# Kernel optimization log

Hardware: AMD Instinct MI355X
Metric: run time of the kernel (lower is better)

The kernel has to match this reference:

```python
import jax, jax.numpy as jnp
import numpy as np

H, W = 512, 512          # pseudo_image_dims
C = 32                   # feat_channels == MHA embed_dim
NH, HD = 2, 16           # heads, head_dim
B, NL, NR = 2, 50000, 20000
EPS = 1e-5
SCALE = np.float32(1.0 / np.sqrt(HD))

# 3x3 neighbor shifts used by shift_bev_grids (INDEX_SHIFT in source)
INDEX_SHIFT = jnp.array([[0, 0], [-1, 0], [1, 0], [0, 1], [-1, 1], [1, 1], [0, -1], [-1, -1], [1, -1]], dtype=jnp.int32)
# 5x5 shifts used by new_gen_dy_coor (gen_index_shift(2))
SHIFT25 = jnp.array([[i, j] for i in range(-2, 3) for j in range(-2, 3)], dtype=jnp.int32)


def _unique_coords(key, n):
    perm = jax.random.permutation(key, H * W)[:n]
    return jnp.stack([perm // W, perm % W], axis=1).astype(jnp.int32)


def setup_inputs():
    key = jax.random.key(0)
    ks = jax.random.split(key, 8)
    inp = {
        "li_bev_feats": jax.random.normal(ks[0], (B, NL, C), jnp.float32),
        "li_bev_coors": jnp.stack([_unique_coords(jax.random.fold_in(ks[1], b), NL) for b in range(B)]),
        "ra_bev_feats": jax.random.normal(ks[2], (B, NR, C), jnp.float32),
        "ra_bev_coors": jnp.stack([_unique_coords(jax.random.fold_in(ks[3], b), NR) for b in range(B)]),
        "radar_bev_dy": jax.random.bernoulli(ks[4], 0.3, (B, NR)),
    }
    pk = jax.random.split(ks[5], 12)
    w = lambda k, o, i: 0.05 * jax.random.normal(k, (o, i), jnp.float32)
    z = lambda n: jnp.zeros((n,), jnp.float32)
    inp.update(
        ln_li_w=jnp.ones((C,), jnp.float32), ln_li_b=z(C),
        ln_ra_w=jnp.ones((C,), jnp.float32), ln_ra_b=z(C),
        q1_w=w(pk[0], C, C), q1_b=z(C), k1_w=w(pk[1], C, C), k1_b=z(C), v1_w=w(pk[2], C, C), v1_b=z(C),
        q2_w=w(pk[3], C, C), q2_b=z(C), k2_w=w(pk[4], C, C), k2_b=z(C), v2_w=w(pk[5], C, C), v2_b=z(C),
        pos_w=w(pk[6], C, 2), pos_b=z(C),
        a1_in_w=w(pk[7], 3 * C, C), a1_in_b=z(3 * C), a1_out_w=w(pk[8], C, C), a1_out_b=z(C),
        a2_in_w=w(pk[9], 3 * C, C), a2_in_b=z(3 * C), a2_out_w=w(pk[10], C, C), a2_out_b=z(C),
    )
    return inp


def _ln(x, w, b):
    mu = jnp.mean(x, -1, keepdims=True)
    var = jnp.mean(jnp.square(x - mu), -1, keepdims=True)
    return (x - mu) / jnp.sqrt(var + EPS) * w + b


def _grid_of(coors, n):
    # dense coord -> pillar-index lookup table, -1 for empty cells
    return jnp.full((H, W), -1, jnp.int32).at[coors[:, 0], coors[:, 1]].set(jnp.arange(n, dtype=jnp.int32))


def _gather_kv(coors, grid, k_map, v_map, pe9):
    # per pillar: look up the 3x3 shifted neighbors in the OTHER modality's grid
    sh = coors[:, None, :] + INDEX_SHIFT[None]                      # [N,9,2]
    inb = (sh[..., 0] >= 0) & (sh[..., 0] < H) & (sh[..., 1] >= 0) & (sh[..., 1] < W)
    idx = grid[jnp.clip(sh[..., 0], 0, H - 1), jnp.clip(sh[..., 1], 0, W - 1)]
    valid = (inb & (idx >= 0))[..., None]                           # [N,9,1]
    safe = jnp.clip(idx, 0, None)
    k = jnp.where(valid, k_map[safe], 0.0)                          # masked_fill(~cond, 0)
    v = jnp.where(valid, v_map[safe] + pe9[None], 0.0)              # pos-enc added before masking
    return k, v


def _mha(q, k, v, Wi, bi, Wo, bo):
    # torch MultiheadAttention (batch_first, eval -> no dropout); q [N,1,C], k/v [N,9,C]
    n = q.shape[0]
    qp = (q @ Wi[:C].T + bi[:C]).reshape(n, 1, NH, HD)
    kp = (k @ Wi[C:2 * C].T + bi[C:2 * C]).reshape(n, -1, NH, HD)
    vp = (v @ Wi[2 * C:].T + bi[2 * C:]).reshape(n, -1, NH, HD)
    s = jnp.einsum("nqhd,nkhd->nhqk", qp, kp) * SCALE
    a = jax.nn.softmax(s, axis=-1)
    o = jnp.einsum("nhqk,nkhd->nqhd", a, vp).reshape(n, C)
    return o @ Wo.T + bo


def _scatter(coors, feat):
    # PointPillarsScatter: place [N,C] features at their (x,y) cells of a [C,H,W] canvas
    return jnp.zeros((H, W, C), feat.dtype).at[coors[:, 0], coors[:, 1]].set(feat).transpose(2, 0, 1)


def _forward(li_bev_feats, li_bev_coors, ra_bev_feats, ra_bev_coors, radar_bev_dy,
             ln_li_w, ln_li_b, ln_ra_w, ln_ra_b,
             q1_w, q1_b, k1_w, k1_b, v1_w, v1_b,
             q2_w, q2_b, k2_w, k2_b, v2_w, v2_b,
             pos_w, pos_b,
             a1_in_w, a1_in_b, a1_out_w, a1_out_b,
             a2_in_w, a2_in_b, a2_out_w, a2_out_b):
    pe9 = INDEX_SHIFT.astype(jnp.float32) @ pos_w.T + pos_b        # [9,C] positional codes

    def per_sample(li_f, li_c, ra_f, ra_c, ra_dy):
        li_n = _ln(li_f, ln_li_w, ln_li_b)
        ra_n = _ln(ra_f, ln_ra_w, ln_ra_b)
        li_grid = _grid_of(li_c, NL)
        ra_grid = _grid_of(ra_c, NR)
        # new_gen_dy_coor: lidar pillars within a 5x5 (mod dims+1) window of any dynamic radar pillar
        g = jnp.array([H + 1, W + 1], jnp.int32)
        sh = (ra_c[:, None, :] + SHIFT25[None]) % g                # [NR,25,2]
        inb = (sh[..., 0] < H) & (sh[..., 1] < W)
        idx = li_grid[jnp.clip(sh[..., 0], 0, H - 1), jnp.clip(sh[..., 1], 0, W - 1)]
        valid = inb & (idx >= 0) & ra_dy[:, None]
        dy_mask = jnp.zeros(NL + 1, bool).at[jnp.where(valid, idx, NL).reshape(-1)].set(True)[:NL]
        # branch 1: dynamic lidar queries cross-attend to 3x3 radar neighbors
        q1 = li_n @ q1_w.T + q1_b
        k1 = ra_n @ k1_w.T + k1_b
        v1 = ra_n @ v1_w.T + v1_b
        k, v = _gather_kv(li_c, ra_grid, k1, v1, pe9)
        out1 = _mha(q1[:, None, :], k, v, a1_in_w, a1_in_b, a1_out_w, a1_out_b)
        out1 = out1 * dy_mask[:, None].astype(out1.dtype)          # only dy pillars scattered
        img_li = _scatter(li_c, out1)
        # branch 2: radar queries cross-attend to 3x3 lidar neighbors
        q2 = ra_n @ q2_w.T + q2_b
        k2 = li_n @ k2_w.T + k2_b
        v2 = li_n @ v2_w.T + v2_b
        k, v = _gather_kv(ra_c, li_grid, k2, v2, pe9)
        out2 = _mha(q2[:, None, :], k, v, a2_in_w, a2_in_b, a2_out_w, a2_out_b)
        img_ra = _scatter(ra_c, out2)
        return img_li, img_ra

    return jax.vmap(per_sample)(li_bev_feats, li_bev_coors, ra_bev_feats, ra_bev_coors, radar_bev_dy)


def reference(li_bev_feats, li_bev_coors, ra_bev_feats, ra_bev_coors, radar_bev_dy,
              ln_li_w, ln_li_b, ln_ra_w, ln_ra_b,
              q1_w, q1_b, k1_w, k1_b, v1_w, v1_b,
              q2_w, q2_b, k2_w, k2_b, v2_w, v2_b,
              pos_w, pos_b,
              a1_in_w, a1_in_b, a1_out_w, a1_out_b,
              a2_in_w, a2_in_b, a2_out_w, a2_out_b):
    return _forward(li_bev_feats, li_bev_coors, ra_bev_feats, ra_bev_coors, radar_bev_dy,
                    ln_li_w, ln_li_b, ln_ra_w, ln_ra_b,
                    q1_w, q1_b, k1_w, k1_b, v1_w, v1_b,
                    q2_w, q2_b, k2_w, k2_b, v2_w, v2_b,
                    pos_w, pos_b,
                    a1_in_w, a1_in_b, a1_out_w, a1_out_b,
                    a2_in_w, a2_in_b, a2_out_w, a2_out_b)
```

## Files before the change

kernel.cpp:

```cpp
#include <hip/hip_runtime.h>
#include <stdint.h>

constexpr int Hh = 512, Ww = 512;
constexpr int HW = Hh * Ww;
constexpr int C  = 32;
constexpr int B  = 2;
constexpr int NL = 50000;
constexpr int NR = 20000;
constexpr float EPS = 1e-5f;
constexpr float SCALE = 0.25f;

constexpr int GBL = (NL + NR + 255) / 256;
constexpr int LB  = (NL + 255) / 256;
constexpr int RB  = (NR + 255) / 256;

constexpr int CB_MATS = 0;
constexpr int CB_CVEC = 6144;
constexpr int CB_PE1  = 6336;
constexpr int CB_PE2  = 6624;
constexpr int CB_INV  = 6912;
constexpr int CB_TOT  = 7040;

__device__ __constant__ int DX9[9] = {0,-1,1,0,-1,1,0,-1,1};
__device__ __constant__ int DY9[9] = {0,0,0,1,1,1,-1,-1,-1};

__global__ void setup_k(const int* __restrict__ li_c, const int* __restrict__ ra_c,
                        const int* __restrict__ ra_dy,
                        int* __restrict__ li_grid, int* __restrict__ ra_grid,
                        uint8_t* __restrict__ rdy_grid,
                        const float* __restrict__ a1w, const float* __restrict__ a1b,
                        const float* __restrict__ a2w, const float* __restrict__ a2b,
                        const float* __restrict__ q1w, const float* __restrict__ q1b,
                        const float* __restrict__ k1w, const float* __restrict__ k1b,
                        const float* __restrict__ v1w, const float* __restrict__ v1b,
                        const float* __restrict__ q2w, const float* __restrict__ q2b,
                        const float* __restrict__ k2w, const float* __restrict__ k2b,
                        const float* __restrict__ v2w, const float* __restrict__ v2b,
                        const float* __restrict__ posw, const float* __restrict__ posb,
                        float* __restrict__ cb) {
    int bx = blockIdx.x, b = blockIdx.y, t = threadIdx.x;
    if (bx < GBL) {
        int i = bx * 256 + t;
        if (i < NL) {
            int x = li_c[((size_t)b * NL + i) * 2 + 0];
            int y = li_c[((size_t)b * NL + i) * 2 + 1];
            li_grid[(size_t)b * HW + x * Ww + y] = i;
        } else if (i < NL + NR) {
            int j = i - NL;
            int x = ra_c[((size_t)b * NR + j) * 2 + 0];
            int y = ra_c[((size_t)b * NR + j) * 2 + 1];
            ra_grid[(size_t)b * HW + x * Ww + y] = j;
            if (ra_dy[(size_t)b * NR + j] != 0)
                rdy_grid[(size_t)b * HW + x * Ww + y] = 0;
        }
        return;
    }
    if (b != 0) return;
    if (bx < GBL + 6) {
        int m = bx - GBL;
        const float* A = (m < 3 ? a1w : a2w) + (m % 3) * C * C;
        const float* Wm;
        switch (m) { case 0: Wm=q1w; break; case 1: Wm=k1w; break; case 2: Wm=v1w; break;
                     case 3: Wm=q2w; break; case 4: Wm=k2w; break; default: Wm=v2w; }
        for (int p = t; p < 1024; p += 256) {
            int r = p >> 5, d = p & 31;
            float s = 0.f;
            #pragma unroll
            for (int c = 0; c < C; ++c) s += A[r * C + c] * Wm[c * C + d];
            cb[CB_MATS + m * 1024 + r * C + d] = s;
        }
        return;
    }
    for (int u = t; u < 896; u += 256) {
        if (u < 192) {
            int mm = u / 32, r = u & 31;
            const float* A  = (mm < 3 ? a1w : a2w) + (mm % 3) * C * C;
            const float* ab = (mm < 3 ? a1b : a2b) + (mm % 3) * C;
            const float* bv = (mm == 0 ? q1b : mm == 1 ? k1b : mm == 2 ? v1b
                             : mm == 3 ? q2b : mm == 4 ? k2b : v2b);
            float s = ab[r];
            #pragma unroll
            for (int c = 0; c < C; ++c) s += A[r * C + c] * bv[c];
            cb[CB_CVEC + mm * 32 + r] = s;
        } else if (u < 768) {
            int w = u - 192;
            int br = w / 288; int v = w % 288; int j = v >> 5, r = v & 31;
            const float* A = (br == 0 ? a1w : a2w) + 2 * C * C;
            float sx = (float)DX9[j], sy = (float)DY9[j];
            float s = 0.f;
            #pragma unroll
            for (int c = 0; c < C; ++c) {
                float pe = posw[c * 2 + 0] * sx + posw[c * 2 + 1] * sy + posb[c];
                s += A[r * C + c] * pe;
            }
            cb[(br == 0 ? CB_PE1 : CB_PE2) + j * 32 + r] = s;
        } else {
            int v = u - 768; int mm = v >> 5, r = v & 31;
            cb[CB_INV + v] = (mm == 0 ? a1b[32 + r] : mm == 1 ? a1b[64 + r]
                            : mm == 2 ? a2b[32 + r] : a2b[64 + r]);
        }
    }
}

__global__ void ln_proj_k(const float* __restrict__ li_f, const float* __restrict__ ra_f,
                          const float* __restrict__ ln_li_w, const float* __restrict__ ln_li_b,
                          const float* __restrict__ ln_ra_w, const float* __restrict__ ln_ra_b,
                          const float* __restrict__ cb,
                          float* __restrict__ qp1, float* __restrict__ kp2, float* __restrict__ vp2,
                          float* __restrict__ qp2, float* __restrict__ kp1, float* __restrict__ vp1) {
    bool lidar = (blockIdx.x < LB);
    int n  = lidar ? NL : NR;
    int i  = (lidar ? blockIdx.x : blockIdx.x - LB) * 256 + threadIdx.x;
    int b  = blockIdx.y;
    int mq = lidar ? 0 : 3, mk = lidar ? 4 : 1, mv = lidar ? 5 : 2;
    const float* feats = lidar ? li_f : ra_f;
    const float* lnw = lidar ? ln_li_w : ln_ra_w;
    const float* lnb = lidar ? ln_li_b : ln_ra_b;
    float* o0 = lidar ? qp1 : qp2;
    float* o1 = lidar ? kp2 : kp1;
    float* o2 = lidar ? vp2 : vp1;

    __shared__ float sM[3][1024];
    __shared__ float sc[3][32];
    for (int p = threadIdx.x; p < 1024; p += blockDim.x) {
        sM[0][p] = cb[CB_MATS + mq * 1024 + p];
        sM[1][p] = cb[CB_MATS + mk * 1024 + p];
        sM[2][p] = cb[CB_MATS + mv * 1024 + p];
    }
    if (threadIdx.x < 32) {
        sc[0][threadIdx.x] = cb[CB_CVEC + mq * 32 + threadIdx.x];
        sc[1][threadIdx.x] = cb[CB_CVEC + mk * 32 + threadIdx.x];
        sc[2][threadIdx.x] = cb[CB_CVEC + mv * 32 + threadIdx.x];
    }
    __syncthreads();
    if (i >= n) return;

    float x[C];
    const float4* f4 = (const float4*)(feats + ((size_t)b * n + i) * C);
    #pragma unroll
    for (int q = 0; q < 8; ++q) {
        float4 t = f4[q];
        x[4*q] = t.x; x[4*q+1] = t.y; x[4*q+2] = t.z; x[4*q+3] = t.w;
    }
    float mu = 0.f;
    #pragma unroll
    for (int c = 0; c < C; ++c) mu += x[c];
    mu *= (1.0f / C);
    float var = 0.f;
    #pragma unroll
    for (int c = 0; c < C; ++c) { float d = x[c] - mu; var += d * d; }
    var *= (1.0f / C);
    float inv = 1.0f / sqrtf(var + EPS);
    #pragma unroll
    for (int c = 0; c < C; ++c) x[c] = (x[c] - mu) * inv * lnw[c] + lnb[c];

    float* outs[3] = { o0, o1, o2 };
    #pragma unroll
    for (int m = 0; m < 3; ++m) {
        float4* o4 = (float4*)(outs[m] + ((size_t)b * n + i) * C);
        #pragma unroll
        for (int rq = 0; rq < 8; ++rq) {
            float4 t;
            float* tp = &t.x;
            #pragma unroll
            for (int rr = 0; rr < 4; ++rr) {
                int r = rq * 4 + rr;
                float s = sc[m][r];
                #pragma unroll
                for (int d = 0; d < C; ++d) s += sM[m][r * C + d] * x[d];
                tp[rr] = s;
            }
            o4[rq] = t;
        }
    }
}

__global__ void attn_k(const float* __restrict__ qp1, const float* __restrict__ kp1,
                       const float* __restrict__ vp1, const float* __restrict__ qp2,
                       const float* __restrict__ kp2, const float* __restrict__ vp2,
                       const int* __restrict__ li_c, const int* __restrict__ ra_c,
                       const int* __restrict__ li_grid, const int* __restrict__ ra_grid,
                       const uint8_t* __restrict__ rdy_grid, const float* __restrict__ cb,
                       const float* __restrict__ a1ow, const float* __restrict__ a1ob,
                       const float* __restrict__ a2ow, const float* __restrict__ a2ob,
                       float* __restrict__ feat1, float* __restrict__ feat2) {
    bool br1 = (blockIdx.x < LB);
    int nq  = br1 ? NL : NR;
    int nkv = br1 ? NR : NL;
    int i   = (br1 ? blockIdx.x : blockIdx.x - LB) * 256 + threadIdx.x;
    int b   = blockIdx.y;
    const float* qmap = br1 ? qp1 : qp2;
    const float* kmap = br1 ? kp1 : kp2;
    const float* vmap = br1 ? vp1 : vp2;
    const int* q_coors  = br1 ? li_c : ra_c;
    const int* kv_grid  = br1 ? ra_grid : li_grid;
    const float* Wo = br1 ? a1ow : a2ow;
    const float* bo = br1 ? a1ob : a2ob;
    int pe_off   = br1 ? CB_PE1 : CB_PE2;
    int kinv_off = br1 ? CB_INV + 0  : CB_INV + 64;
    int vinv_off = br1 ? CB_INV + 32 : CB_INV + 96;
    float* feat  = br1 ? feat1 : feat2;

    __shared__ float sWo[1024];
    __shared__ float sbo[32], skinv[32], svinv[32];
    __shared__ float spe[9 * 32];
    for (int p = threadIdx.x; p < 1024; p += blockDim.x) sWo[p] = Wo[p];
    if (threadIdx.x < 32) {
        sbo[threadIdx.x]   = bo[threadIdx.x];
        skinv[threadIdx.x] = cb[kinv_off + threadIdx.x];
        svinv[threadIdx.x] = cb[vinv_off + threadIdx.x];
    }
    for (int p = threadIdx.x; p < 288; p += blockDim.x) spe[p] = cb[pe_off + p];
    __syncthreads();

    if (i >= nq) return;
    float4* o4 = (float4*)(feat + ((size_t)b * nq + i) * C);

    int x = q_coors[((size_t)b * nq + i) * 2 + 0];
    int y = q_coors[((size_t)b * nq + i) * 2 + 1];

    if (br1) {
        bool dy = false;
        #pragma unroll
        for (int dx = -2; dx <= 2 && !dy; ++dx) {
            int cx = x + dx;
            cx = (cx < 0) ? cx + 513 : (cx >= 513 ? cx - 513 : cx);
            if (cx == 512) continue;
            #pragma unroll
            for (int dyy = -2; dyy <= 2; ++dyy) {
                int cy = y + dyy;
                cy = (cy < 0) ? cy + 513 : (cy >= 513 ? cy - 513 : cy);
                if (cy == 512) continue;
                if (rdy_grid[(size_t)b * HW + cx * Ww + cy] == 0) { dy = true; break; }
            }
        }
        if (!dy) {
            float4 z = {0.f, 0.f, 0.f, 0.f};
            #pragma unroll
            for (int q = 0; q < 8; ++q) o4[q] = z;
            return;
        }
    }

    int nidx[9];
    #pragma unroll
    for (int j = 0; j < 9; ++j) {
        int sx = x + DX9[j], sy = y + DY9[j];
        nidx[j] = (sx >= 0 && sx < Hh && sy >= 0 && sy < Ww)
                  ? kv_grid[(size_t)b * HW + sx * Ww + sy] : -1;
    }

    float qp[C];
    const float4* qp4 = (const float4*)(qmap + ((size_t)b * nq + i) * C);
    #pragma unroll
    for (int q = 0; q < 8; ++q) {
        float4 t = qp4[q];
        qp[4*q] = t.x; qp[4*q+1] = t.y; qp[4*q+2] = t.z; qp[4*q+3] = t.w;
    }

    float sc0[9], sc1[9];
    #pragma unroll
    for (int j = 0; j < 9; ++j) {
        int idx = nidx[j];
        const float4* kp4 = (idx >= 0) ? (const float4*)(kmap + ((size_t)b * nkv + idx) * C)
                                       : (const float4*)skinv;
        float s0 = 0.f, s1 = 0.f;
        #pragma unroll
        for (int q = 0; q < 4; ++q) {
            float4 t = kp4[q];
            s0 += qp[4*q] * t.x + qp[4*q+1] * t.y + qp[4*q+2] * t.z + qp[4*q+3] * t.w;
        }
        #pragma unroll
        for (int q = 4; q < 8; ++q) {
            float4 t = kp4[q];
            s1 += qp[4*q] * t.x + qp[4*q+1] * t.y + qp[4*q+2] * t.z + qp[4*q+3] * t.w;
        }
        sc0[j] = s0 * SCALE; sc1[j] = s1 * SCALE;
    }
    float m0 = sc0[0], m1 = sc1[0];
    #pragma unroll
    for (int j = 1; j < 9; ++j) { m0 = fmaxf(m0, sc0[j]); m1 = fmaxf(m1, sc1[j]); }
    float sum0 = 0.f, sum1 = 0.f;
    #pragma unroll
    for (int j = 0; j < 9; ++j) {
        sc0[j] = expf(sc0[j] - m0); sum0 += sc0[j];
        sc1[j] = expf(sc1[j] - m1); sum1 += sc1[j];
    }
    float r0 = 1.0f / sum0, r1 = 1.0f / sum1;

    float o[C];
    #pragma unroll
    for (int c = 0; c < C; ++c) o[c] = 0.f;
    #pragma unroll
    for (int j = 0; j < 9; ++j) {
        float a0 = sc0[j] * r0, a1 = sc1[j] * r1;
        int idx = nidx[j];
        if (idx >= 0) {
            const float4* vp4 = (const float4*)(vmap + ((size_t)b * nkv + idx) * C);
            #pragma unroll
            for (int q = 0; q < 8; ++q) {
                float4 t = vp4[q];
                float a = (q < 4) ? a0 : a1;
                o[4*q]   += a * (t.x + spe[j * 32 + 4*q]);
                o[4*q+1] += a * (t.y + spe[j * 32 + 4*q+1]);
                o[4*q+2] += a * (t.z + spe[j * 32 + 4*q+2]);
                o[4*q+3] += a * (t.w + spe[j * 32 + 4*q+3]);
            }
        } else {
            #pragma unroll
            for (int d = 0; d < 16; ++d) {
                o[d]      += a0 * svinv[d];
                o[16 + d] += a1 * svinv[16 + d];
            }
        }
    }

    #pragma unroll
    for (int rq = 0; rq < 8; ++rq) {
        float4 t;
        float* tp = &t.x;
        #pragma unroll
        for (int rr = 0; rr < 4; ++rr) {
            int r = rq * 4 + rr;
            float s = sbo[r];
            #pragma unroll
            for (int c = 0; c < C; ++c) s += sWo[r * C + c] * o[c];
            tp[rr] = s;
        }
        o4[rq] = t;
    }
}

__global__ void canvas_k(const int* __restrict__ li_grid, const int* __restrict__ ra_grid,
                         const float* __restrict__ feat1, const float* __restrict__ feat2,
                         float* __restrict__ out_li, float* __restrict__ out_ra) {
    int b = blockIdx.y;
    int cell = blockIdx.x * blockDim.x + threadIdx.x;
    if (cell >= HW) return;
    size_t gidx = (size_t)b * HW + cell;
    size_t obase = (size_t)b * C * HW + cell;

    int li = li_grid[gidx];
    float v[C];
    if (li >= 0) {
        const float4* f = (const float4*)(feat1 + ((size_t)b * NL + li) * C);
        #pragma unroll
        for (int q = 0; q < 8; ++q) {
            float4 t = f[q];
            v[4*q] = t.x; v[4*q+1] = t.y; v[4*q+2] = t.z; v[4*q+3] = t.w;
        }
    } else {
        #pragma unroll
        for (int c = 0; c < C; ++c) v[c] = 0.f;
    }
    #pragma unroll
    for (int c = 0; c < C; ++c) out_li[obase + (size_t)c * HW] = v[c];

    int ra = ra_grid[gidx];
    if (ra >= 0) {
        const float4* f = (const float4*)(feat2 + ((size_t)b * NR + ra) * C);
        #pragma unroll
        for (int q = 0; q < 8; ++q) {
            float4 t = f[q];
            v[4*q] = t.x; v[4*q+1] = t.y; v[4*q+2] = t.z; v[4*q+3] = t.w;
        }
    } else {
        #pragma unroll
        for (int c = 0; c < C; ++c) v[c] = 0.f;
    }
    #pragma unroll
    for (int c = 0; c < C; ++c) out_ra[obase + (size_t)c * HW] = v[c];
}

extern "C" void kernel_launch(void* const* d_in, const int* in_sizes, int n_in,
                              void* d_out, int out_size, void* d_ws, size_t ws_size,
                              hipStream_t stream) {
    const float*   li_f  = (const float*)d_in[0];
    const int*     li_c  = (const int*)d_in[1];
    const float*   ra_f  = (const float*)d_in[2];
    const int*     ra_c  = (const int*)d_in[3];
    const int*     ra_dy = (const int*)d_in[4];
    const float* ln_li_w = (const float*)d_in[5];
    const float* ln_li_b = (const float*)d_in[6];
    const float* ln_ra_w = (const float*)d_in[7];
    const float* ln_ra_b = (const float*)d_in[8];
    const float* q1w = (const float*)d_in[9],  *q1b = (const float*)d_in[10];
    const float* k1w = (const float*)d_in[11], *k1b = (const float*)d_in[12];
    const float* v1w = (const float*)d_in[13], *v1b = (const float*)d_in[14];
    const float* q2w = (const float*)d_in[15], *q2b = (const float*)d_in[16];
    const float* k2w = (const float*)d_in[17], *k2b = (const float*)d_in[18];
    const float* v2w = (const float*)d_in[19], *v2b = (const float*)d_in[20];
    const float* posw = (const float*)d_in[21], *posb = (const float*)d_in[22];
    const float* a1iw = (const float*)d_in[23], *a1ib = (const float*)d_in[24];
    const float* a1ow = (const float*)d_in[25], *a1ob = (const float*)d_in[26];
    const float* a2iw = (const float*)d_in[27], *a2ib = (const float*)d_in[28];
    const float* a2ow = (const float*)d_in[29], *a2ob = (const float*)d_in[30];

    char* ws = (char*)d_ws;
    size_t off = 0;
    auto carve = [&](size_t bytes) { void* p = ws + off; off += (bytes + 255) & ~(size_t)255; return p; };
    int*     li_grid  = (int*)carve((size_t)B * HW * 4);
    int*     ra_grid  = (int*)carve((size_t)B * HW * 4);
    uint8_t* rdy_grid = (uint8_t*)carve((size_t)B * HW);
    size_t   init_bytes = off;
    float*   cb    = (float*)carve((size_t)CB_TOT * 4);
    float*   qp1   = (float*)carve((size_t)B * NL * C * 4);
    float*   kp1   = (float*)carve((size_t)B * NR * C * 4);
    float*   vp1   = (float*)carve((size_t)B * NR * C * 4);
    float*   qp2   = (float*)carve((size_t)B * NR * C * 4);
    float*   kp2   = (float*)carve((size_t)B * NL * C * 4);
    float*   vp2   = (float*)carve((size_t)B * NL * C * 4);
    float*   feat1 = (float*)carve((size_t)B * NL * C * 4);
    float*   feat2 = (float*)carve((size_t)B * NR * C * 4);
    (void)ws_size; (void)n_in; (void)in_sizes; (void)out_size;

    float* out_li = (float*)d_out;
    float* out_ra = out_li + (size_t)B * C * HW;

    hipMemsetAsync(li_grid, 0xFF, init_bytes, stream);

    setup_k<<<dim3(GBL + 7, B), dim3(256), 0, stream>>>(
        li_c, ra_c, ra_dy, li_grid, ra_grid, rdy_grid,
        a1iw, a1ib, a2iw, a2ib, q1w, q1b, k1w, k1b, v1w, v1b,
        q2w, q2b, k2w, k2b, v2w, v2b, posw, posb, cb);

    ln_proj_k<<<dim3(LB + RB, B), dim3(256), 0, stream>>>(
        li_f, ra_f, ln_li_w, ln_li_b, ln_ra_w, ln_ra_b, cb,
        qp1, kp2, vp2, qp2, kp1, vp1);

    attn_k<<<dim3(LB + RB, B), dim3(256), 0, stream>>>(
        qp1, kp1, vp1, qp2, kp2, vp2, li_c, ra_c, li_grid, ra_grid, rdy_grid, cb,
        a1ow, a1ob, a2ow, a2ob, feat1, feat2);

    canvas_k<<<dim3((HW + 255) / 256, B), dim3(256), 0, stream>>>(
        li_grid, ra_grid, feat1, feat2, out_li, out_ra);
}
```

Measured before the change: 331.9 us.

## Fuse setup into projection and attention into canvas scatter kernel

```diff
diff --git a/kernel.cpp b/kernel.cpp
--- a/kernel.cpp
+++ b/kernel.cpp
@@ -14,30 +14,26 @@
 constexpr int LB  = (NL + 255) / 256;
 constexpr int RB  = (NR + 255) / 256;
 
-constexpr int CB_MATS = 0;
-constexpr int CB_CVEC = 6144;
-constexpr int CB_PE1  = 6336;
-constexpr int CB_PE2  = 6624;
-constexpr int CB_INV  = 6912;
-constexpr int CB_TOT  = 7040;
-
 __device__ __constant__ int DX9[9] = {0,-1,1,0,-1,1,0,-1,1};
 __device__ __constant__ int DY9[9] = {0,0,0,1,1,1,-1,-1,-1};
 
-__global__ void setup_k(const int* __restrict__ li_c, const int* __restrict__ ra_c,
-                        const int* __restrict__ ra_dy,
-                        int* __restrict__ li_grid, int* __restrict__ ra_grid,
-                        uint8_t* __restrict__ rdy_grid,
-                        const float* __restrict__ a1w, const float* __restrict__ a1b,
-                        const float* __restrict__ a2w, const float* __restrict__ a2b,
-                        const float* __restrict__ q1w, const float* __restrict__ q1b,
-                        const float* __restrict__ k1w, const float* __restrict__ k1b,
-                        const float* __restrict__ v1w, const float* __restrict__ v1b,
-                        const float* __restrict__ q2w, const float* __restrict__ q2b,
-                        const float* __restrict__ k2w, const float* __restrict__ k2b,
-                        const float* __restrict__ v2w, const float* __restrict__ v2b,
-                        const float* __restrict__ posw, const float* __restrict__ posb,
-                        float* __restrict__ cb) {
+__global__ void build_proj_k(const int* __restrict__ li_c, const int* __restrict__ ra_c,
+                             const int* __restrict__ ra_dy,
+                             int* __restrict__ li_grid, int* __restrict__ ra_grid,
+                             uint8_t* __restrict__ rdy_grid,
+                             const float* __restrict__ li_f, const float* __restrict__ ra_f,
+                             const float* __restrict__ ln_li_w, const float* __restrict__ ln_li_b,
+                             const float* __restrict__ ln_ra_w, const float* __restrict__ ln_ra_b,
+                             const float* __restrict__ a1iw, const float* __restrict__ a1ib,
+                             const float* __restrict__ a2iw, const float* __restrict__ a2ib,
+                             const float* __restrict__ q1w, const float* __restrict__ q1b,
+                             const float* __restrict__ k1w, const float* __restrict__ k1b,
+                             const float* __restrict__ v1w, const float* __restrict__ v1b,
+                             const float* __restrict__ q2w, const float* __restrict__ q2b,
+                             const float* __restrict__ k2w, const float* __restrict__ k2b,
+                             const float* __restrict__ v2w, const float* __restrict__ v2b,
+                             float* __restrict__ qp1, float* __restrict__ kp1, float* __restrict__ vp1,
+                             float* __restrict__ qp2, float* __restrict__ kp2, float* __restrict__ vp2) {
     int bx = blockIdx.x, b = blockIdx.y, t = threadIdx.x;
     if (bx < GBL) {
         int i = bx * 256 + t;
@@ -55,82 +51,38 @@
         }
         return;
     }
-    if (b != 0) return;
-    if (bx < GBL + 6) {
-        int m = bx - GBL;
-        const float* A = (m < 3 ? a1w : a2w) + (m % 3) * C * C;
-        const float* Wm;
-        switch (m) { case 0: Wm=q1w; break; case 1: Wm=k1w; break; case 2: Wm=v1w; break;
-                     case 3: Wm=q2w; break; case 4: Wm=k2w; break; default: Wm=v2w; }
-        for (int p = t; p < 1024; p += 256) {
-            int r = p >> 5, d = p & 31;
-            float s = 0.f;
-            #pragma unroll
-            for (int c = 0; c < C; ++c) s += A[r * C + c] * Wm[c * C + d];
-            cb[CB_MATS + m * 1024 + r * C + d] = s;
-        }
-        return;
-    }
-    for (int u = t; u < 896; u += 256) {
-        if (u < 192) {
-            int mm = u / 32, r = u & 31;
-            const float* A  = (mm < 3 ? a1w : a2w) + (mm % 3) * C * C;
-            const float* ab = (mm < 3 ? a1b : a2b) + (mm % 3) * C;
-            const float* bv = (mm == 0 ? q1b : mm == 1 ? k1b : mm == 2 ? v1b
-                             : mm == 3 ? q2b : mm == 4 ? k2b : v2b);
-            float s = ab[r];
-            #pragma unroll
-            for (int c = 0; c < C; ++c) s += A[r * C + c] * bv[c];
-            cb[CB_CVEC + mm * 32 + r] = s;
-        } else if (u < 768) {
-            int w = u - 192;
-            int br = w / 288; int v = w % 288; int j = v >> 5, r = v & 31;
-            const float* A = (br == 0 ? a1w : a2w) + 2 * C * C;
-            float sx = (float)DX9[j], sy = (float)DY9[j];
-            float s = 0.f;
-            #pragma unroll
-            for (int c = 0; c < C; ++c) {
-                float pe = posw[c * 2 + 0] * sx + posw[c * 2 + 1] * sy + posb[c];
-                s += A[r * C + c] * pe;
-            }
-            cb[(br == 0 ? CB_PE1 : CB_PE2) + j * 32 + r] = s;
-        } else {
-            int v = u - 768; int mm = v >> 5, r = v & 31;
-            cb[CB_INV + v] = (mm == 0 ? a1b[32 + r] : mm == 1 ? a1b[64 + r]
-                            : mm == 2 ? a2b[32 + r] : a2b[64 + r]);
-        }
-    }
-}
-
-__global__ void ln_proj_k(const float* __restrict__ li_f, const float* __restrict__ ra_f,
-                          const float* __restrict__ ln_li_w, const float* __restrict__ ln_li_b,
-                          const float* __restrict__ ln_ra_w, const float* __restrict__ ln_ra_b,
-                          const float* __restrict__ cb,
-                          float* __restrict__ qp1, float* __restrict__ kp2, float* __restrict__ vp2,
-                          float* __restrict__ qp2, float* __restrict__ kp1, float* __restrict__ vp1) {
-    bool lidar = (blockIdx.x < LB);
-    int n  = lidar ? NL : NR;
-    int i  = (lidar ? blockIdx.x : blockIdx.x - LB) * 256 + threadIdx.x;
-    int b  = blockIdx.y;
-    int mq = lidar ? 0 : 3, mk = lidar ? 4 : 1, mv = lidar ? 5 : 2;
+
+    bool lidar = (bx - GBL < LB);
+    int n = lidar ? NL : NR;
+    int i = (lidar ? bx - GBL : bx - GBL - LB) * 256 + t;
     const float* feats = lidar ? li_f : ra_f;
     const float* lnw = lidar ? ln_li_w : ln_ra_w;
     const float* lnb = lidar ? ln_li_b : ln_ra_b;
-    float* o0 = lidar ? qp1 : qp2;
-    float* o1 = lidar ? kp2 : kp1;
-    float* o2 = lidar ? vp2 : vp1;
+    const float* Asec[3] = { (lidar ? a1iw : a2iw) + 0 * C * C,
+                             (lidar ? a2iw : a1iw) + 1 * C * C,
+                             (lidar ? a2iw : a1iw) + 2 * C * C };
+    const float* absec[3] = { (lidar ? a1ib : a2ib) + 0 * C,
+                              (lidar ? a2ib : a1ib) + 1 * C,
+                              (lidar ? a2ib : a1ib) + 2 * C };
+    const float* Wsec[3] = { lidar ? q1w : q2w, lidar ? k2w : k1w, lidar ? v2w : v1w };
+    const float* bsec[3] = { lidar ? q1b : q2b, lidar ? k2b : k1b, lidar ? v2b : v1b };
+    float* outp[3] = { lidar ? qp1 : qp2, lidar ? kp2 : kp1, lidar ? vp2 : vp1 };
 
     __shared__ float sM[3][1024];
     __shared__ float sc[3][32];
-    for (int p = threadIdx.x; p < 1024; p += blockDim.x) {
-        sM[0][p] = cb[CB_MATS + mq * 1024 + p];
-        sM[1][p] = cb[CB_MATS + mk * 1024 + p];
-        sM[2][p] = cb[CB_MATS + mv * 1024 + p];
-    }
-    if (threadIdx.x < 32) {
-        sc[0][threadIdx.x] = cb[CB_CVEC + mq * 32 + threadIdx.x];
-        sc[1][threadIdx.x] = cb[CB_CVEC + mk * 32 + threadIdx.x];
-        sc[2][threadIdx.x] = cb[CB_CVEC + mv * 32 + threadIdx.x];
+    for (int p = t; p < 3072; p += 256) {
+        int m = p >> 10, e = p & 1023, r = e >> 5, d = e & 31;
+        float s = 0.f;
+        #pragma unroll
+        for (int c = 0; c < C; ++c) s += Asec[m][r * C + c] * Wsec[m][c * C + d];
+        sM[m][e] = s;
+    }
+    if (t < 96) {
+        int m = t >> 5, r = t & 31;
+        float s = absec[m][r];
+        #pragma unroll
+        for (int c = 0; c < C; ++c) s += Asec[m][r * C + c] * bsec[m][c];
+        sc[m][r] = s;
     }
     __syncthreads();
     if (i >= n) return;
@@ -139,8 +91,8 @@
     const float4* f4 = (const float4*)(feats + ((size_t)b * n + i) * C);
     #pragma unroll
     for (int q = 0; q < 8; ++q) {
-        float4 t = f4[q];
-        x[4*q] = t.x; x[4*q+1] = t.y; x[4*q+2] = t.z; x[4*q+3] = t.w;
+        float4 tv = f4[q];
+        x[4*q] = tv.x; x[4*q+1] = tv.y; x[4*q+2] = tv.z; x[4*q+3] = tv.w;
     }
     float mu = 0.f;
     #pragma unroll
@@ -154,14 +106,13 @@
     #pragma unroll
     for (int c = 0; c < C; ++c) x[c] = (x[c] - mu) * inv * lnw[c] + lnb[c];
 
-    float* outs[3] = { o0, o1, o2 };
     #pragma unroll
     for (int m = 0; m < 3; ++m) {
-        float4* o4 = (float4*)(outs[m] + ((size_t)b * n + i) * C);
+        float4* o4 = (float4*)(outp[m] + ((size_t)b * n + i) * C);
         #pragma unroll
         for (int rq = 0; rq < 8; ++rq) {
-            float4 t;
-            float* tp = &t.x;
+            float4 tv;
+            float* tp = &tv.x;
             #pragma unroll
             for (int rr = 0; rr < 4; ++rr) {
                 int r = rq * 4 + rr;
@@ -170,59 +121,148 @@
                 for (int d = 0; d < C; ++d) s += sM[m][r * C + d] * x[d];
                 tp[rr] = s;
             }
-            o4[rq] = t;
+            o4[rq] = tv;
         }
     }
 }
 
-__global__ void attn_k(const float* __restrict__ qp1, const float* __restrict__ kp1,
-                       const float* __restrict__ vp1, const float* __restrict__ qp2,
-                       const float* __restrict__ kp2, const float* __restrict__ vp2,
-                       const int* __restrict__ li_c, const int* __restrict__ ra_c,
-                       const int* __restrict__ li_grid, const int* __restrict__ ra_grid,
-                       const uint8_t* __restrict__ rdy_grid, const float* __restrict__ cb,
-                       const float* __restrict__ a1ow, const float* __restrict__ a1ob,
-                       const float* __restrict__ a2ow, const float* __restrict__ a2ob,
-                       float* __restrict__ feat1, float* __restrict__ feat2) {
-    bool br1 = (blockIdx.x < LB);
-    int nq  = br1 ? NL : NR;
-    int nkv = br1 ? NR : NL;
-    int i   = (br1 ? blockIdx.x : blockIdx.x - LB) * 256 + threadIdx.x;
-    int b   = blockIdx.y;
-    const float* qmap = br1 ? qp1 : qp2;
-    const float* kmap = br1 ? kp1 : kp2;
-    const float* vmap = br1 ? vp1 : vp2;
-    const int* q_coors  = br1 ? li_c : ra_c;
-    const int* kv_grid  = br1 ? ra_grid : li_grid;
-    const float* Wo = br1 ? a1ow : a2ow;
-    const float* bo = br1 ? a1ob : a2ob;
-    int pe_off   = br1 ? CB_PE1 : CB_PE2;
-    int kinv_off = br1 ? CB_INV + 0  : CB_INV + 64;
-    int vinv_off = br1 ? CB_INV + 32 : CB_INV + 96;
-    float* feat  = br1 ? feat1 : feat2;
-
-    __shared__ float sWo[1024];
-    __shared__ float sbo[32], skinv[32], svinv[32];
-    __shared__ float spe[9 * 32];
-    for (int p = threadIdx.x; p < 1024; p += blockDim.x) sWo[p] = Wo[p];
-    if (threadIdx.x < 32) {
-        sbo[threadIdx.x]   = bo[threadIdx.x];
-        skinv[threadIdx.x] = cb[kinv_off + threadIdx.x];
-        svinv[threadIdx.x] = cb[vinv_off + threadIdx.x];
-    }
-    for (int p = threadIdx.x; p < 288; p += blockDim.x) spe[p] = cb[pe_off + p];
+__device__ __forceinline__ void attn_cell(
+        int x, int y, int nkv,
+        const float* __restrict__ qrow,
+        const float* __restrict__ kmap, const float* __restrict__ vmap,
+        const int* __restrict__ kv_grid,
+        const float* sWo, const float* sbo, const float* spe,
+        const float* skinv, const float* svinv,
+        float* v) {
+    int nidx[9];
+    #pragma unroll
+    for (int j = 0; j < 9; ++j) {
+        int sx = x + DX9[j], sy = y + DY9[j];
+        nidx[j] = (sx >= 0 && sx < Hh && sy >= 0 && sy < Ww) ? kv_grid[sx * Ww + sy] : -1;
+    }
+    float qp[C];
+    const float4* qp4 = (const float4*)qrow;
+    #pragma unroll
+    for (int q = 0; q < 8; ++q) {
+        float4 tv = qp4[q];
+        qp[4*q] = tv.x; qp[4*q+1] = tv.y; qp[4*q+2] = tv.z; qp[4*q+3] = tv.w;
+    }
+    float sc0[9], sc1[9];
+    #pragma unroll
+    for (int j = 0; j < 9; ++j) {
+        int idx = nidx[j];
+        const float4* kp4 = (idx >= 0) ? (const float4*)(kmap + (size_t)idx * C)
+                                       : (const float4*)skinv;
+        float s0 = 0.f, s1 = 0.f;
+        #pragma unroll
+        for (int q = 0; q < 4; ++q) {
+            float4 tv = kp4[q];
+            s0 += qp[4*q] * tv.x + qp[4*q+1] * tv.y + qp[4*q+2] * tv.z + qp[4*q+3] * tv.w;
+        }
+        #pragma unroll
+        for (int q = 4; q < 8; ++q) {
+            float4 tv = kp4[q];
+            s1 += qp[4*q] * tv.x + qp[4*q+1] * tv.y + qp[4*q+2] * tv.z + qp[4*q+3] * tv.w;
+        }
+        sc0[j] = s0 * SCALE; sc1[j] = s1 * SCALE;
+    }
+    float m0 = sc0[0], m1 = sc1[0];
+    #pragma unroll
+    for (int j = 1; j < 9; ++j) { m0 = fmaxf(m0, sc0[j]); m1 = fmaxf(m1, sc1[j]); }
+    float sum0 = 0.f, sum1 = 0.f;
+    #pragma unroll
+    for (int j = 0; j < 9; ++j) {
+        sc0[j] = expf(sc0[j] - m0); sum0 += sc0[j];
+        sc1[j] = expf(sc1[j] - m1); sum1 += sc1[j];
+    }
+    float r0 = 1.0f / sum0, r1 = 1.0f / sum1;
+
+    float o[C];
+    #pragma unroll
+    for (int c = 0; c < C; ++c) o[c] = 0.f;
+    #pragma unroll
+    for (int j = 0; j < 9; ++j) {
+        float a0 = sc0[j] * r0, a1 = sc1[j] * r1;
+        int idx = nidx[j];
+        if (idx >= 0) {
+            const float4* vp4 = (const float4*)(vmap + (size_t)idx * C);
+            #pragma unroll
+            for (int q = 0; q < 8; ++q) {
+                float4 tv = vp4[q];
+                float a = (q < 4) ? a0 : a1;
+                o[4*q]   += a * (tv.x + spe[j * 32 + 4*q]);
+                o[4*q+1] += a * (tv.y + spe[j * 32 + 4*q+1]);
+                o[4*q+2] += a * (tv.z + spe[j * 32 + 4*q+2]);
+                o[4*q+3] += a * (tv.w + spe[j * 32 + 4*q+3]);
+            }
+        } else {
+            #pragma unroll
+            for (int d = 0; d < 16; ++d) {
+                o[d]      += a0 * svinv[d];
+                o[16 + d] += a1 * svinv[16 + d];
+            }
+        }
+    }
+    #pragma unroll
+    for (int r = 0; r < C; ++r) {
+        float s = sbo[r];
+        #pragma unroll
+        for (int c = 0; c < C; ++c) s += sWo[r * C + c] * o[c];
+        v[r] = s;
+    }
+}
+
+__global__ void attn_canvas_k(const int* __restrict__ li_grid, const int* __restrict__ ra_grid,
+                              const uint8_t* __restrict__ rdy_grid,
+                              const float* __restrict__ qp1, const float* __restrict__ kp1,
+                              const float* __restrict__ vp1, const float* __restrict__ qp2,
+                              const float* __restrict__ kp2, const float* __restrict__ vp2,
+                              const float* __restrict__ a1iw, const float* __restrict__ a1ib,
+                              const float* __restrict__ a2iw, const float* __restrict__ a2ib,
+                              const float* __restrict__ posw, const float* __restrict__ posb,
+                              const float* __restrict__ a1ow, const float* __restrict__ a1ob,
+                              const float* __restrict__ a2ow, const float* __restrict__ a2ob,
+                              float* __restrict__ out_li, float* __restrict__ out_ra) {
+    __shared__ alignas(16) float sWo1[1024], sWo2[1024];
+    __shared__ alignas(16) float sbo1[32], sbo2[32];
+    __shared__ alignas(16) float spe1[288], spe2[288];
+    __shared__ alignas(16) float skinv1[32], svinv1[32], skinv2[32], svinv2[32];
+    int t = threadIdx.x;
+    for (int p = t; p < 1024; p += 256) { sWo1[p] = a1ow[p]; sWo2[p] = a2ow[p]; }
+    if (t < 32) {
+        sbo1[t] = a1ob[t]; sbo2[t] = a2ob[t];
+        skinv1[t] = a1ib[32 + t]; svinv1[t] = a1ib[64 + t];
+        skinv2[t] = a2ib[32 + t]; svinv2[t] = a2ib[64 + t];
+    }
+    for (int p = t; p < 576; p += 256) {
+        int br = p / 288; int e = p % 288; int j = e >> 5, r = e & 31;
+        const float* Av = (br == 0 ? a1iw : a2iw) + 2 * C * C;
+        float sx = (float)DX9[j], sy = (float)DY9[j];
+        float s = 0.f;
+        #pragma unroll
+        for (int c = 0; c < C; ++c) {
+            float pe = posw[c * 2 + 0] * sx + posw[c * 2 + 1] * sy + posb[c];
+            s += Av[r * C + c] * pe;
+        }
+        (br == 0 ? spe1 : spe2)[e] = s;
+    }
     __syncthreads();
 
-    if (i >= nq) return;
-    float4* o4 = (float4*)(feat + ((size_t)b * nq + i) * C);
-
-    int x = q_coors[((size_t)b * nq + i) * 2 + 0];
-    int y = q_coors[((size_t)b * nq + i) * 2 + 1];
-
-    if (br1) {
-        bool dy = false;
-        #pragma unroll
-        for (int dx = -2; dx <= 2 && !dy; ++dx) {
+    int b = blockIdx.y;
+    int cell = blockIdx.x * 256 + t;
+    int x = cell >> 9, y = cell & 511;
+    size_t gidx = (size_t)b * HW + cell;
+    size_t obase = (size_t)b * C * HW + cell;
+
+    int li = li_grid[gidx];
+    int ra = ra_grid[gidx];
+    const uint8_t* rdy = rdy_grid + (size_t)b * HW;
+
+    float v[C];
+    bool do1 = false;
+    if (li >= 0) {
+        #pragma unroll
+        for (int dx = -2; dx <= 2 && !do1; ++dx) {
             int cx = x + dx;
             cx = (cx < 0) ? cx + 513 : (cx >= 513 ? cx - 513 : cx);
             if (cx == 512) continue;
@@ -231,124 +271,14 @@
                 int cy = y + dyy;
                 cy = (cy < 0) ? cy + 513 : (cy >= 513 ? cy - 513 : cy);
                 if (cy == 512) continue;
-                if (rdy_grid[(size_t)b * HW + cx * Ww + cy] == 0) { dy = true; break; }
+                if (rdy[cx * Ww + cy] == 0) { do1 = true; break; }
             }
         }
-        if (!dy) {
-            float4 z = {0.f, 0.f, 0.f, 0.f};
-            #pragma unroll
-            for (int q = 0; q < 8; ++q) o4[q] = z;
-            return;
-        }
-    }
-
-    int nidx[9];
-    #pragma unroll
-    for (int j = 0; j < 9; ++j) {
-        int sx = x + DX9[j], sy = y + DY9[j];
-        nidx[j] = (sx >= 0 && sx < Hh && sy >= 0 && sy < Ww)
-                  ? kv_grid[(size_t)b * HW + sx * Ww + sy] : -1;
-    }
-
-    float qp[C];
-    const float4* qp4 = (const float4*)(qmap + ((size_t)b * nq + i) * C);
-    #pragma unroll
-    for (int q = 0; q < 8; ++q) {
-        float4 t = qp4[q];
-        qp[4*q] = t.x; qp[4*q+1] = t.y; qp[4*q+2] = t.z; qp[4*q+3] = t.w;
-    }
-
-    float sc0[9], sc1[9];
-    #pragma unroll
-    for (int j = 0; j < 9; ++j) {
-        int idx = nidx[j];
-        const float4* kp4 = (idx >= 0) ? (const float4*)(kmap + ((size_t)b * nkv + idx) * C)
-                                       : (const float4*)skinv;
-        float s0 = 0.f, s1 = 0.f;
-        #pragma unroll
-        for (int q = 0; q < 4; ++q) {
-            float4 t = kp4[q];
-            s0 += qp[4*q] * t.x + qp[4*q+1] * t.y + qp[4*q+2] * t.z + qp[4*q+3] * t.w;
-        }
-        #pragma unroll
-        for (int q = 4; q < 8; ++q) {
-            float4 t = kp4[q];
-            s1 += qp[4*q] * t.x + qp[4*q+1] * t.y + qp[4*q+2] * t.z + qp[4*q+3] * t.w;
-        }
-        sc0[j] = s0 * SCALE; sc1[j] = s1 * SCALE;
-    }
-    float m0 = sc0[0], m1 = sc1[0];
-    #pragma unroll
-    for (int j = 1; j < 9; ++j) { m0 = fmaxf(m0, sc0[j]); m1 = fmaxf(m1, sc1[j]); }
-    float sum0 = 0.f, sum1 = 0.f;
-    #pragma unroll
-    for (int j = 0; j < 9; ++j) {
-        sc0[j] = expf(sc0[j] - m0); sum0 += sc0[j];
-        sc1[j] = expf(sc1[j] - m1); sum1 += sc1[j];
-    }
-    float r0 = 1.0f / sum0, r1 = 1.0f / sum1;
-
-    float o[C];
-    #pragma unroll
-    for (int c = 0; c < C; ++c) o[c] = 0.f;
-    #pragma unroll
-    for (int j = 0; j < 9; ++j) {
-        float a0 = sc0[j] * r0, a1 = sc1[j] * r1;
-        int idx = nidx[j];
-        if (idx >= 0) {
-            const float4* vp4 = (const float4*)(vmap + ((size_t)b * nkv + idx) * C);
-            #pragma unroll
-            for (int q = 0; q < 8; ++q) {
-                float4 t = vp4[q];
-                float a = (q < 4) ? a0 : a1;
-                o[4*q]   += a * (t.x + spe[j * 32 + 4*q]);
-                o[4*q+1] += a * (t.y + spe[j * 32 + 4*q+1]);
-                o[4*q+2] += a * (t.z + spe[j * 32 + 4*q+2]);
-                o[4*q+3] += a * (t.w + spe[j * 32 + 4*q+3]);
-            }
-        } else {
-            #pragma unroll
-            for (int d = 0; d < 16; ++d) {
-                o[d]      += a0 * svinv[d];
-                o[16 + d] += a1 * svinv[16 + d];
-            }
-        }
-    }
-
-    #pragma unroll
-    for (int rq = 0; rq < 8; ++rq) {
-        float4 t;
-        float* tp = &t.x;
-        #pragma unroll
-        for (int rr = 0; rr < 4; ++rr) {
-            int r = rq * 4 + rr;
-            float s = sbo[r];
-            #pragma unroll
-            for (int c = 0; c < C; ++c) s += sWo[r * C + c] * o[c];
-            tp[rr] = s;
-        }
-        o4[rq] = t;
-    }
-}
-
-__global__ void canvas_k(const int* __restrict__ li_grid, const int* __restrict__ ra_grid,
-                         const float* __restrict__ feat1, const float* __restrict__ feat2,
-                         float* __restrict__ out_li, float* __restrict__ out_ra) {
-    int b = blockIdx.y;
-    int cell = blockIdx.x * blockDim.x + threadIdx.x;
-    if (cell >= HW) return;
-    size_t gidx = (size_t)b * HW + cell;
-    size_t obase = (size_t)b * C * HW + cell;
-
-    int li = li_grid[gidx];
-    float v[C];
-    if (li >= 0) {
-        const float4* f = (const float4*)(feat1 + ((size_t)b * NL + li) * C);
-        #pragma unroll
-        for (int q = 0; q < 8; ++q) {
-            float4 t = f[q];
-            v[4*q] = t.x; v[4*q+1] = t.y; v[4*q+2] = t.z; v[4*q+3] = t.w;
-        }
+    }
+    if (do1) {
+        attn_cell(x, y, NR, qp1 + ((size_t)b * NL + li) * C,
+                  kp1 + (size_t)b * NR * C, vp1 + (size_t)b * NR * C,
+                  ra_grid + (size_t)b * HW, sWo1, sbo1, spe1, skinv1, svinv1, v);
     } else {
         #pragma unroll
         for (int c = 0; c < C; ++c) v[c] = 0.f;
@@ -356,14 +286,10 @@
     #pragma unroll
     for (int c = 0; c < C; ++c) out_li[obase + (size_t)c * HW] = v[c];
 
-    int ra = ra_grid[gidx];
     if (ra >= 0) {
-        const float4* f = (const float4*)(feat2 + ((size_t)b * NR + ra) * C);
-        #pragma unroll
-        for (int q = 0; q < 8; ++q) {
-            float4 t = f[q];
-            v[4*q] = t.x; v[4*q+1] = t.y; v[4*q+2] = t.z; v[4*q+3] = t.w;
-        }
+        attn_cell(x, y, NL, qp2 + ((size_t)b * NR + ra) * C,
+                  kp2 + (size_t)b * NL * C, vp2 + (size_t)b * NL * C,
+                  li_grid + (size_t)b * HW, sWo2, sbo2, spe2, skinv2, svinv2, v);
     } else {
         #pragma unroll
         for (int c = 0; c < C; ++c) v[c] = 0.f;
@@ -403,15 +329,12 @@
     int*     ra_grid  = (int*)carve((size_t)B * HW * 4);
     uint8_t* rdy_grid = (uint8_t*)carve((size_t)B * HW);
     size_t   init_bytes = off;
-    float*   cb    = (float*)carve((size_t)CB_TOT * 4);
-    float*   qp1   = (float*)carve((size_t)B * NL * C * 4);
-    float*   kp1   = (float*)carve((size_t)B * NR * C * 4);
-    float*   vp1   = (float*)carve((size_t)B * NR * C * 4);
-    float*   qp2   = (float*)carve((size_t)B * NR * C * 4);
-    float*   kp2   = (float*)carve((size_t)B * NL * C * 4);
-    float*   vp2   = (float*)carve((size_t)B * NL * C * 4);
-    float*   feat1 = (float*)carve((size_t)B * NL * C * 4);
-    float*   feat2 = (float*)carve((size_t)B * NR * C * 4);
+    float*   qp1 = (float*)carve((size_t)B * NL * C * 4);
+    float*   kp1 = (float*)carve((size_t)B * NR * C * 4);
+    float*   vp1 = (float*)carve((size_t)B * NR * C * 4);
+    float*   qp2 = (float*)carve((size_t)B * NR * C * 4);
+    float*   kp2 = (float*)carve((size_t)B * NL * C * 4);
+    float*   vp2 = (float*)carve((size_t)B * NL * C * 4);
     (void)ws_size; (void)n_in; (void)in_sizes; (void)out_size;
 
     float* out_li = (float*)d_out;
@@ -419,19 +342,15 @@
 
     hipMemsetAsync(li_grid, 0xFF, init_bytes, stream);
 
-    setup_k<<<dim3(GBL + 7, B), dim3(256), 0, stream>>>(
+    build_proj_k<<<dim3(GBL + LB + RB, B), dim3(256), 0, stream>>>(
         li_c, ra_c, ra_dy, li_grid, ra_grid, rdy_grid,
-        a1iw, a1ib, a2iw, a2ib, q1w, q1b, k1w, k1b, v1w, v1b,
-        q2w, q2b, k2w, k2b, v2w, v2b, posw, posb, cb);
-
-    ln_proj_k<<<dim3(LB + RB, B), dim3(256), 0, stream>>>(
-        li_f, ra_f, ln_li_w, ln_li_b, ln_ra_w, ln_ra_b, cb,
-        qp1, kp2, vp2, qp2, kp1, vp1);
-
-    attn_k<<<dim3(LB + RB, B), dim3(256), 0, stream>>>(
-        qp1, kp1, vp1, qp2, kp2, vp2, li_c, ra_c, li_grid, ra_grid, rdy_grid, cb,
-        a1ow, a1ob, a2ow, a2ob, feat1, feat2);
-
-    canvas_k<<<dim3((HW + 255) / 256, B), dim3(256), 0, stream>>>(
-        li_grid, ra_grid, feat1, feat2, out_li, out_ra);
+        li_f, ra_f, ln_li_w, ln_li_b, ln_ra_w, ln_ra_b,
+        a1iw, a1ib, a2iw, a2ib,
+        q1w, q1b, k1w, k1b, v1w, v1b, q2w, q2b, k2w, k2b, v2w, v2b,
+        qp1, kp1, vp1, qp2, kp2, vp2);
+
+    attn_canvas_k<<<dim3(HW / 256, B), dim3(256), 0, stream>>>(
+        li_grid, ra_grid, rdy_grid, qp1, kp1, vp1, qp2, kp2, vp2,
+        a1iw, a1ib, a2iw, a2ib, posw, posb, a1ow, a1ob, a2ow, a2ob,
+        out_li, out_ra);
 }
```

Result: slower. 553.4 us (+66.7%).
